# Kernel optimization log

Measured on AMD Instinct MI355X. Metric: run time of the kernel, lower is better.

## Reference

```python
import jax, jax.numpy as jnp
import numpy as np

B, T, IN, H = 64, 2048, 9, 128
FC1, OUT = 20, 1


def setup_inputs() -> dict:
    key = jax.random.key(0)
    ks = jax.random.split(key, 13)
    sh = 1.0 / np.sqrt(H)  # torch LSTM/Linear default init scale ~ U(-1/sqrt(H), 1/sqrt(H)); use gaussian of same magnitude
    s20 = 1.0 / np.sqrt(FC1)
    n = lambda k, shape, sc: (jax.random.normal(k, shape, jnp.float32) * sc)
    return {
        "x": jax.random.normal(ks[0], (B, T, IN), jnp.float32),
        # layer 0: W_ih [4H, IN], W_hh [4H, H]  (torch gate order: i, f, g, o)
        "W_ih0": n(ks[1], (4 * H, IN), sh),
        "W_hh0": n(ks[2], (4 * H, H), sh),
        "b_ih0": n(ks[3], (4 * H,), sh),
        "b_hh0": n(ks[4], (4 * H,), sh),
        # layer 1: input is h of layer 0 -> W_ih [4H, H]
        "W_ih1": n(ks[5], (4 * H, H), sh),
        "W_hh1": n(ks[6], (4 * H, H), sh),
        "b_ih1": n(ks[7], (4 * H,), sh),
        "b_hh1": n(ks[8], (4 * H,), sh),
        # head: fc1 (H->20), fc2 (20->1)
        "fc1_w": n(ks[9], (FC1, H), sh),
        "fc1_b": n(ks[10], (FC1,), sh),
        "fc2_w": n(ks[11], (OUT, FC1), s20),
        "fc2_b": n(ks[12], (OUT,), s20),
    }


def _lstm_layer(x, W_ih, W_hh, b_ih, b_hh):
    # x: [B, T, D_in] -> h_seq: [B, T, H]. Zero initial state (as in the module).
    b, t, _ = x.shape
    h_dim = W_hh.shape[1]
    # Precompute input-to-gate GEMM over all timesteps at once: [B, T, 4H]
    xg = jnp.einsum('btd,gd->btg', x, W_ih) + b_ih + b_hh

    def step(carry, g_t):  # g_t: [B, 4H]
        h, c = carry
        g = g_t + h @ W_hh.T
        i, f, gg, o = jnp.split(g, 4, axis=-1)
        i = jax.nn.sigmoid(i)
        f = jax.nn.sigmoid(f)
        gg = jnp.tanh(gg)
        o = jax.nn.sigmoid(o)
        c = f * c + i * gg
        h = o * jnp.tanh(c)
        return (h, c), h

    h0 = jnp.zeros((b, h_dim), x.dtype)
    c0 = jnp.zeros((b, h_dim), x.dtype)
    _, hs = jax.lax.scan(step, (h0, c0), jnp.swapaxes(xg, 0, 1))  # hs: [T, B, H]
    return jnp.swapaxes(hs, 0, 1)


def reference(x, W_ih0, W_hh0, b_ih0, b_hh0, W_ih1, W_hh1, b_ih1, b_hh1,
              fc1_w, fc1_b, fc2_w, fc2_b):
    out = _lstm_layer(x, W_ih0, W_hh0, b_ih0, b_hh0)
    out = _lstm_layer(out, W_ih1, W_hh1, b_ih1, b_hh1)
    # Per-timestep head fused into single batched GEMMs over all (B*T) rows.
    # Dropout(0.5) is identity in eval mode.
    h = jnp.tanh(out @ fc1_w.T + fc1_b)          # [B, T, 20]
    real_out = h @ fc2_w.T + fc2_b               # [B, T, 1]
    return real_out
```

## Files before the change

### kernel.cpp

```cpp
#include <hip/hip_runtime.h>
#include <hip/hip_bf16.h>

#define BATCH 64
#define TSEQ 2048
#define INF 9
#define H 128
#define G4 512
#define NFC 20
#define CH 64
#define NCH (TSEQ / CH)

__device__ __forceinline__ float sigf(float x) {
    return 1.0f / (1.0f + __expf(-x));
}
__device__ __forceinline__ float tanh_fast(float x) {
    return 1.0f - 2.0f / (__expf(2.0f * x) + 1.0f);
}

__device__ __forceinline__ void flag_release(int* f) {
    if (threadIdx.x == 0) {
        __threadfence();
        __hip_atomic_store(f, 1, __ATOMIC_RELEASE, __HIP_MEMORY_SCOPE_AGENT);
    }
}
__device__ __forceinline__ void flag_acquire(int* f) {
    if (threadIdx.x == 0) {
        while (__hip_atomic_load(f, __ATOMIC_ACQUIRE, __HIP_MEMORY_SCOPE_AGENT) == 0)
            __builtin_amdgcn_s_sleep(32);
        __threadfence();
    }
    __syncthreads();
}

__global__ __launch_bounds__(512) void zero_flags(int* flags, int n) {
    for (int i = threadIdx.x; i < n; i += 512) flags[i] = 0;
}

__global__ __launch_bounds__(512) void lstm_fused(
    const float* __restrict__ x,
    const float* __restrict__ Wih0, const float* __restrict__ Whh0,
    const float* __restrict__ bih0, const float* __restrict__ bhh0,
    const float* __restrict__ Wih1, const float* __restrict__ Whh1,
    const float* __restrict__ bih1, const float* __restrict__ bhh1,
    const float* __restrict__ fc1w, const float* __restrict__ fc1b,
    const float* __restrict__ fc2w, const float* __restrict__ fc2b,
    float* __restrict__ h0ring, float* __restrict__ xgring,
    int* __restrict__ fA, int* __restrict__ fAfree,
    int* __restrict__ fB, int* __restrict__ fBfree,
    int R, float* __restrict__ out)
{
    __shared__ float hs[H];
    __shared__ float gates[G4];
    __shared__ float hsB[2][H];
    __shared__ float hbuf[64][132];
    __shared__ float fc1w_s[NFC * 132];
    __shared__ float hfcb[64 * NFC];
    __shared__ float fc2w_s[NFC];
    __shared__ float fc1b_s[NFC];

    const int role = blockIdx.x >> 6;
    const int b    = blockIdx.x & 63;
    const int g    = threadIdx.x;

    if (role == 0) {
        float wih[INF], whh[H];
#pragma unroll
        for (int k = 0; k < INF; k++) wih[k] = Wih0[(size_t)g * INF + k];
        const float4* W4 = (const float4*)(Whh0 + (size_t)g * H);
#pragma unroll
        for (int k4 = 0; k4 < H / 4; k4++) {
            float4 wv = W4[k4];
            whh[4 * k4 + 0] = wv.x; whh[4 * k4 + 1] = wv.y;
            whh[4 * k4 + 2] = wv.z; whh[4 * k4 + 3] = wv.w;
        }
        const float bias = bih0[g] + bhh0[g];

        float c = 0.f;
        if (g < H) hs[g] = 0.f;

        const float* xb = x + (size_t)b * TSEQ * INF;
        float xr[INF];
#pragma unroll
        for (int k = 0; k < INF; k++) xr[k] = xb[k];
        __syncthreads();

        for (int ci = 0; ci < NCH; ci++) {
            if (ci >= R) flag_acquire(&fAfree[b * NCH + ci - R]);
            const int slot = ci % R;
            float* h0s = h0ring + ((size_t)slot * BATCH + b) * CH * H;

            for (int tt = 0; tt < CH; tt++) {
                const int t = ci * CH + tt;
                float a0 = bias, a1 = 0.f, a2 = 0.f, a3 = 0.f;
#pragma unroll
                for (int k = 0; k < INF; k++) a0 += wih[k] * xr[k];
                if (t + 1 < TSEQ) {
                    const float* xn = xb + (size_t)(t + 1) * INF;
#pragma unroll
                    for (int k = 0; k < INF; k++) xr[k] = xn[k];
                }
                const float4* h4 = (const float4*)hs;
#pragma unroll
                for (int k4 = 0; k4 < H / 4; k4++) {
                    float4 hv = h4[k4];
                    a0 += whh[4 * k4 + 0] * hv.x;
                    a1 += whh[4 * k4 + 1] * hv.y;
                    a2 += whh[4 * k4 + 2] * hv.z;
                    a3 += whh[4 * k4 + 3] * hv.w;
                }
                gates[g] = (a0 + a1) + (a2 + a3);
                __syncthreads();
                if (g < H) {
                    float ig = sigf(gates[g]);
                    float fg = sigf(gates[H + g]);
                    float gg = tanh_fast(gates[2 * H + g]);
                    float og = sigf(gates[3 * H + g]);
                    c = fg * c + ig * gg;
                    float h = og * tanh_fast(c);
                    hs[g] = h;
                    h0s[(size_t)tt * H + g] = h;
                }
                __syncthreads();
            }
            flag_release(&fA[b * NCH + ci]);
        }
    } else if (role == 1) {
        const float bias = bih1[g] + bhh1[g];
        const float4* W4 = (const float4*)(Wih1 + (size_t)g * H);

        for (int ci = 0; ci < NCH; ci++) {
            flag_acquire(&fA[b * NCH + ci]);
            if (ci >= R) flag_acquire(&fBfree[b * NCH + ci - R]);
            const int slot = ci % R;
            const float* h0s = h0ring + ((size_t)slot * BATCH + b) * CH * H;
            float* xgs = xgring + ((size_t)slot * BATCH + b) * CH * G4;

            for (int r2 = 0; r2 < CH / 2; r2++) {
                const int tt = 2 * r2;
                if (g < H)
                    hsB[0][g] = h0s[(size_t)tt * H + g];
                else if (g < 2 * H)
                    hsB[1][g - H] = h0s[(size_t)(tt + 1) * H + (g - H)];
                __syncthreads();
                float a0 = bias, a1 = 0.f, a2 = 0.f, a3 = 0.f;
                float c0 = bias, c1 = 0.f, c2 = 0.f, c3 = 0.f;
                const float4* h40 = (const float4*)hsB[0];
                const float4* h41 = (const float4*)hsB[1];
#pragma unroll
                for (int k4 = 0; k4 < H / 4; k4++) {
                    float4 wv = W4[k4];
                    float4 hv0 = h40[k4];
                    float4 hv1 = h41[k4];
                    a0 += wv.x * hv0.x; a1 += wv.y * hv0.y;
                    a2 += wv.z * hv0.z; a3 += wv.w * hv0.w;
                    c0 += wv.x * hv1.x; c1 += wv.y * hv1.y;
                    c2 += wv.z * hv1.z; c3 += wv.w * hv1.w;
                }
                xgs[(size_t)tt * G4 + g]       = (a0 + a1) + (a2 + a3);
                xgs[(size_t)(tt + 1) * G4 + g] = (c0 + c1) + (c2 + c3);
                __syncthreads();
            }
            flag_release(&fAfree[b * NCH + ci]);
            flag_release(&fB[b * NCH + ci]);
        }
    } else {
        float whh[H];
        const float4* W4 = (const float4*)(Whh1 + (size_t)g * H);
#pragma unroll
        for (int k4 = 0; k4 < H / 4; k4++) {
            float4 wv = W4[k4];
            whh[4 * k4 + 0] = wv.x; whh[4 * k4 + 1] = wv.y;
            whh[4 * k4 + 2] = wv.z; whh[4 * k4 + 3] = wv.w;
        }
        for (int i = g; i < NFC * H; i += 512) {
            int r = i >> 7, cidx = i & 127;
            fc1w_s[r * 132 + cidx] = fc1w[i];
        }
        if (g < NFC) { fc2w_s[g] = fc2w[g]; fc1b_s[g] = fc1b[g]; }

        float c = 0.f, h = 0.f;
        if (g < H) hs[g] = 0.f;
        const float fc2bias = fc2b[0];
        __syncthreads();

        for (int ci = 0; ci < NCH; ci++) {
            flag_acquire(&fB[b * NCH + ci]);
            const int slot = ci % R;
            const float* xgs = xgring + ((size_t)slot * BATCH + b) * CH * G4;
            float xgr = xgs[g];

            for (int tt = 0; tt < CH; tt++) {
                float a0 = xgr, a1 = 0.f, a2 = 0.f, a3 = 0.f;
                if (tt + 1 < CH) xgr = xgs[(size_t)(tt + 1) * G4 + g];
                const float4* h4 = (const float4*)hs;
#pragma unroll
                for (int k4 = 0; k4 < H / 4; k4++) {
                    float4 hv = h4[k4];
                    a0 += whh[4 * k4 + 0] * hv.x;
                    a1 += whh[4 * k4 + 1] * hv.y;
                    a2 += whh[4 * k4 + 2] * hv.z;
                    a3 += whh[4 * k4 + 3] * hv.w;
                }
                gates[g] = (a0 + a1) + (a2 + a3);
                __syncthreads();
                if (g < H) {
                    float ig = sigf(gates[g]);
                    float fg = sigf(gates[H + g]);
                    float gg = tanh_fast(gates[2 * H + g]);
                    float og = sigf(gates[3 * H + g]);
                    c = fg * c + ig * gg;
                    h = og * tanh_fast(c);
                    hs[g] = h;
                    hbuf[tt][g] = h;
                }
                __syncthreads();

                if (tt == CH - 1) {
#pragma unroll
                    for (int p = 0; p < 3; p++) {
                        int task = p * 512 + g;
                        if (task < 64 * NFC) {
                            int sidx = task / NFC;
                            int k = task - sidx * NFC;
                            float b0 = fc1b_s[k], b1 = 0.f, b2 = 0.f, b3 = 0.f;
                            const float4* hr = (const float4*)(&hbuf[sidx][0]);
                            const float4* wr = (const float4*)(&fc1w_s[k * 132]);
#pragma unroll
                            for (int k4 = 0; k4 < H / 4; k4++) {
                                float4 hv = hr[k4];
                                float4 wv = wr[k4];
                                b0 += wv.x * hv.x; b1 += wv.y * hv.y;
                                b2 += wv.z * hv.z; b3 += wv.w * hv.w;
                            }
                            hfcb[task] = tanh_fast((b0 + b1) + (b2 + b3));
                        }
                    }
                    __syncthreads();
                    if (g < 64) {
                        float o = fc2bias;
#pragma unroll
                        for (int k = 0; k < NFC; k++) o += fc2w_s[k] * hfcb[g * NFC + k];
                        out[(size_t)b * TSEQ + ci * CH + g] = o;
                    }
                    __syncthreads();
                }
            }
            flag_release(&fBfree[b * NCH + ci]);
        }
    }
}

__global__ __launch_bounds__(512, 2) void lstm0_scan(
    const float* __restrict__ x, const float* __restrict__ Wih,
    const float* __restrict__ Whh, const float* __restrict__ bih,
    const float* __restrict__ bhh, float* __restrict__ h0out)
{
    const int b = blockIdx.x;
    const int g = threadIdx.x;
    __shared__ float hs[H];
    __shared__ float gates[G4];
    float wih[INF], whh[H];
#pragma unroll
    for (int k = 0; k < INF; k++) wih[k] = Wih[(size_t)g * INF + k];
    const float4* W4 = (const float4*)(Whh + (size_t)g * H);
#pragma unroll
    for (int k4 = 0; k4 < H / 4; k4++) {
        float4 wv = W4[k4];
        whh[4 * k4 + 0] = wv.x; whh[4 * k4 + 1] = wv.y;
        whh[4 * k4 + 2] = wv.z; whh[4 * k4 + 3] = wv.w;
    }
    const float bias = bih[g] + bhh[g];
    float c = 0.f;
    if (g < H) hs[g] = 0.f;
    const float* xb = x + (size_t)b * TSEQ * INF;
    float xr[INF];
#pragma unroll
    for (int k = 0; k < INF; k++) xr[k] = xb[k];
    __syncthreads();
    for (int t = 0; t < TSEQ; t++) {
        float a0 = bias, a1 = 0.f, a2 = 0.f, a3 = 0.f;
#pragma unroll
        for (int k = 0; k < INF; k++) a0 += wih[k] * xr[k];
        if (t + 1 < TSEQ) {
            const float* xn = xb + (size_t)(t + 1) * INF;
#pragma unroll
            for (int k = 0; k < INF; k++) xr[k] = xn[k];
        }
        const float4* h4 = (const float4*)hs;
#pragma unroll
        for (int k4 = 0; k4 < H / 4; k4++) {
            float4 hv = h4[k4];
            a0 += whh[4 * k4 + 0] * hv.x;
            a1 += whh[4 * k4 + 1] * hv.y;
            a2 += whh[4 * k4 + 2] * hv.z;
            a3 += whh[4 * k4 + 3] * hv.w;
        }
        gates[g] = (a0 + a1) + (a2 + a3);
        __syncthreads();
        if (g < H) {
            float ig = sigf(gates[g]);
            float fg = sigf(gates[H + g]);
            float gg = tanh_fast(gates[2 * H + g]);
            float og = sigf(gates[3 * H + g]);
            c = fg * c + ig * gg;
            float h = og * tanh_fast(c);
            hs[g] = h;
            h0out[((size_t)b * TSEQ + t) * H + g] = h;
        }
        __syncthreads();
    }
}

__global__ __launch_bounds__(512, 2) void xg1_gemm(
    const float* __restrict__ h0, const float* __restrict__ Wih1,
    const float* __restrict__ bih, const float* __restrict__ bhh,
    float* __restrict__ xg1, int t0, int tlen)
{
    const int b = blockIdx.x >> 2;
    const int s = blockIdx.x & 3;
    const int g = threadIdx.x;
    const int rows = tlen >> 2;
    const int tstart = t0 + s * rows;
    float w[H];
    const float4* W4 = (const float4*)(Wih1 + (size_t)g * H);
#pragma unroll
    for (int k4 = 0; k4 < H / 4; k4++) {
        float4 wv = W4[k4];
        w[4 * k4 + 0] = wv.x; w[4 * k4 + 1] = wv.y;
        w[4 * k4 + 2] = wv.z; w[4 * k4 + 3] = wv.w;
    }
    const float bias = bih[g] + bhh[g];
    __shared__ float hs[2][H];
    if (g < H) hs[0][g] = h0[((size_t)b * TSEQ + tstart) * H + g];
    __syncthreads();
    for (int r = 0; r < rows; r++) {
        int buf = r & 1;
        if (g < H && (r + 1) < rows)
            hs[buf ^ 1][g] = h0[((size_t)b * TSEQ + tstart + r + 1) * H + g];
        float a0 = bias, a1 = 0.f, a2 = 0.f, a3 = 0.f;
        const float4* h4 = (const float4*)hs[buf];
#pragma unroll
        for (int k4 = 0; k4 < H / 4; k4++) {
            float4 hv = h4[k4];
            a0 += w[4 * k4 + 0] * hv.x;
            a1 += w[4 * k4 + 1] * hv.y;
            a2 += w[4 * k4 + 2] * hv.z;
            a3 += w[4 * k4 + 3] * hv.w;
        }
        xg1[((size_t)b * tlen + (size_t)(s * rows + r)) * G4 + g] = (a0 + a1) + (a2 + a3);
        __syncthreads();
    }
}

__global__ __launch_bounds__(512, 2) void lstm1_scan(
    const float* __restrict__ Whh1, const float* __restrict__ xg1,
    const float* __restrict__ fc1w, const float* __restrict__ fc1b,
    const float* __restrict__ fc2w, const float* __restrict__ fc2b,
    float* __restrict__ out, float* __restrict__ state, int t0, int tlen)
{
    const int b = blockIdx.x;
    const int g = threadIdx.x;
    __shared__ float hs[H];
    __shared__ float gates[G4];
    __shared__ float hbuf[64][132];
    __shared__ float fc1w_s[NFC * 132];
    __shared__ float hfcb[64 * NFC];
    __shared__ float fc2w_s[NFC];
    __shared__ float fc1b_s[NFC];
    float whh[H];
    const float4* W4 = (const float4*)(Whh1 + (size_t)g * H);
#pragma unroll
    for (int k4 = 0; k4 < H / 4; k4++) {
        float4 wv = W4[k4];
        whh[4 * k4 + 0] = wv.x; whh[4 * k4 + 1] = wv.y;
        whh[4 * k4 + 2] = wv.z; whh[4 * k4 + 3] = wv.w;
    }
    for (int i = g; i < NFC * H; i += 512) {
        int r = i >> 7, cidx = i & 127;
        fc1w_s[r * 132 + cidx] = fc1w[i];
    }
    if (g < NFC) { fc2w_s[g] = fc2w[g]; fc1b_s[g] = fc1b[g]; }
    float c = 0.f, h = 0.f;
    if (t0 > 0 && g < H) {
        c = state[b * H + g];
        h = state[BATCH * H + b * H + g];
    }
    if (g < H) hs[g] = h;
    float xgr = xg1[((size_t)b * tlen) * G4 + g];
    const float fc2bias = fc2b[0];
    __syncthreads();
    for (int tt = 0; tt < tlen; tt++) {
        float a0 = xgr, a1 = 0.f, a2 = 0.f, a3 = 0.f;
        if (tt + 1 < tlen) xgr = xg1[((size_t)b * tlen + tt + 1) * G4 + g];
        const float4* h4 = (const float4*)hs;
#pragma unroll
        for (int k4 = 0; k4 < H / 4; k4++) {
            float4 hv = h4[k4];
            a0 += whh[4 * k4 + 0] * hv.x;
            a1 += whh[4 * k4 + 1] * hv.y;
            a2 += whh[4 * k4 + 2] * hv.z;
            a3 += whh[4 * k4 + 3] * hv.w;
        }
        gates[g] = (a0 + a1) + (a2 + a3);
        __syncthreads();
        if (g < H) {
            float ig = sigf(gates[g]);
            float fg = sigf(gates[H + g]);
            float gg = tanh_fast(gates[2 * H + g]);
            float og = sigf(gates[3 * H + g]);
            c = fg * c + ig * gg;
            h = og * tanh_fast(c);
            hs[g] = h;
            hbuf[tt & 63][g] = h;
        }
        __syncthreads();
        if ((tt & 63) == 63) {
#pragma unroll
            for (int p = 0; p < 3; p++) {
                int task = p * 512 + g;
                if (task < 64 * NFC) {
                    int sidx = task / NFC;
                    int k = task - sidx * NFC;
                    float b0 = fc1b_s[k], b1 = 0.f, b2 = 0.f, b3 = 0.f;
                    const float4* hr = (const float4*)(&hbuf[sidx][0]);
                    const float4* wr = (const float4*)(&fc1w_s[k * 132]);
#pragma unroll
                    for (int k4 = 0; k4 < H / 4; k4++) {
                        float4 hv = hr[k4];
                        float4 wv = wr[k4];
                        b0 += wv.x * hv.x; b1 += wv.y * hv.y;
                        b2 += wv.z * hv.z; b3 += wv.w * hv.w;
                    }
                    hfcb[task] = tanh_fast((b0 + b1) + (b2 + b3));
                }
            }
            __syncthreads();
            if (g < 64) {
                float o = fc2bias;
#pragma unroll
                for (int k = 0; k < NFC; k++) o += fc2w_s[k] * hfcb[g * NFC + k];
                int tglob = t0 + tt - 63 + g;
                out[(size_t)b * TSEQ + tglob] = o;
            }
            __syncthreads();
        }
    }
    if (g < H) {
        state[b * H + g] = c;
        state[BATCH * H + b * H + g] = h;
    }
}

extern "C" void kernel_launch(void* const* d_in, const int* in_sizes, int n_in,
                              void* d_out, int out_size, void* d_ws, size_t ws_size,
                              hipStream_t stream) {
    const float* x    = (const float*)d_in[0];
    const float* Wih0 = (const float*)d_in[1];
    const float* Whh0 = (const float*)d_in[2];
    const float* bih0 = (const float*)d_in[3];
    const float* bhh0 = (const float*)d_in[4];
    const float* Wih1 = (const float*)d_in[5];
    const float* Whh1 = (const float*)d_in[6];
    const float* bih1 = (const float*)d_in[7];
    const float* bhh1 = (const float*)d_in[8];
    const float* fc1w = (const float*)d_in[9];
    const float* fc1b = (const float*)d_in[10];
    const float* fc2w = (const float*)d_in[11];
    const float* fc2b = (const float*)d_in[12];
    float* out = (float*)d_out;

    char* ws = (char*)d_ws;
    const size_t flag_region = 64 * 1024;
    const size_t h0slot = (size_t)BATCH * CH * H * 4;
    const size_t xgslot = (size_t)BATCH * CH * G4 * 4;

    int R = 0;
    if (ws_size > flag_region)
        R = (int)((ws_size - flag_region) / (h0slot + xgslot));
    if (R > NCH) R = NCH;

    if (R >= 2) {
        int* flags  = (int*)ws;
        int* fAp    = flags;
        int* fAfree = flags + BATCH * NCH;
        int* fBp    = flags + 2 * BATCH * NCH;
        int* fBfree = flags + 3 * BATCH * NCH;
        float* h0ring = (float*)(ws + flag_region);
        float* xgring = (float*)(ws + flag_region + h0slot * (size_t)R);

        zero_flags<<<1, 512, 0, stream>>>(flags, 4 * BATCH * NCH);
        lstm_fused<<<192, 512, 0, stream>>>(x, Wih0, Whh0, bih0, bhh0,
                                            Wih1, Whh1, bih1, bhh1,
                                            fc1w, fc1b, fc2w, fc2b,
                                            h0ring, xgring,
                                            fAp, fAfree, fBp, fBfree,
                                            R, out);
    } else {
        const size_t h0_bytes  = (size_t)BATCH * TSEQ * H * 4;
        const size_t mid_bytes = (size_t)2 * BATCH * H * 4;
        float* h0    = (float*)ws;
        float* state = (float*)(ws + h0_bytes);
        float* xg1   = (float*)(ws + h0_bytes + mid_bytes);
        int tlen = 64;
        const int cands[4] = {2048, 512, 128, 64};
        for (int i = 0; i < 4; i++) {
            size_t need = h0_bytes + mid_bytes + (size_t)BATCH * cands[i] * G4 * 4;
            if (ws_size >= need) { tlen = cands[i]; break; }
        }
        lstm0_scan<<<BATCH, 512, 0, stream>>>(x, Wih0, Whh0, bih0, bhh0, h0);
        const int nch = TSEQ / tlen;
        for (int ci = 0; ci < nch; ci++) {
            xg1_gemm<<<256, 512, 0, stream>>>(h0, Wih1, bih1, bhh1, xg1, ci * tlen, tlen);
            lstm1_scan<<<BATCH, 512, 0, stream>>>(Whh1, xg1, fc1w, fc1b, fc2w, fc2b,
                                                  out, state, ci * tlen, tlen);
        }
    }
}
```

Measured before the change: 3.417 ms.

## Halve pipeline chunk size, batch four timesteps in layer-1 input GEMM

Shrinks the chunk handed between the three pipelined roles from 64 to 32 timesteps, which shortens pipeline fill and drain latency at the cost of twice as many flag handshakes. The layer-1 input projection now processes four timesteps per weight load instead of two, improving weight reuse. Polling sleep is shortened, and the ready flag is released before the free flag so the consumer starts sooner. The head computation still runs every 64 timesteps, tracked by a global step counter, and the flag region and zeroing grid are enlarged to fit the doubled flag count.

```diff
diff --git a/kernel.cpp b/kernel.cpp
--- a/kernel.cpp
+++ b/kernel.cpp
@@ -7,7 +7,7 @@
 #define H 128
 #define G4 512
 #define NFC 20
-#define CH 64
+#define CH 32
 #define NCH (TSEQ / CH)
 
 __device__ __forceinline__ float sigf(float x) {
@@ -26,14 +26,15 @@
 __device__ __forceinline__ void flag_acquire(int* f) {
     if (threadIdx.x == 0) {
         while (__hip_atomic_load(f, __ATOMIC_ACQUIRE, __HIP_MEMORY_SCOPE_AGENT) == 0)
-            __builtin_amdgcn_s_sleep(32);
+            __builtin_amdgcn_s_sleep(2);
         __threadfence();
     }
     __syncthreads();
 }
 
 __global__ __launch_bounds__(512) void zero_flags(int* flags, int n) {
-    for (int i = threadIdx.x; i < n; i += 512) flags[i] = 0;
+    int i = blockIdx.x * 512 + threadIdx.x;
+    for (; i < n; i += gridDim.x * 512) flags[i] = 0;
 }
 
 __global__ __launch_bounds__(512) void lstm_fused(
@@ -51,7 +52,7 @@
 {
     __shared__ float hs[H];
     __shared__ float gates[G4];
-    __shared__ float hsB[2][H];
+    __shared__ float hsB4[4][H];
     __shared__ float hbuf[64][132];
     __shared__ float fc1w_s[NFC * 132];
     __shared__ float hfcb[64 * NFC];
@@ -135,33 +136,34 @@
             const float* h0s = h0ring + ((size_t)slot * BATCH + b) * CH * H;
             float* xgs = xgring + ((size_t)slot * BATCH + b) * CH * G4;
 
-            for (int r2 = 0; r2 < CH / 2; r2++) {
-                const int tt = 2 * r2;
-                if (g < H)
-                    hsB[0][g] = h0s[(size_t)tt * H + g];
-                else if (g < 2 * H)
-                    hsB[1][g - H] = h0s[(size_t)(tt + 1) * H + (g - H)];
+            for (int q = 0; q < CH / 4; q++) {
+                const int tt = 4 * q;
+                {
+                    int r = g >> 7;
+                    int k = g & 127;
+                    hsB4[r][k] = h0s[(size_t)(tt + r) * H + k];
+                }
                 __syncthreads();
-                float a0 = bias, a1 = 0.f, a2 = 0.f, a3 = 0.f;
-                float c0 = bias, c1 = 0.f, c2 = 0.f, c3 = 0.f;
-                const float4* h40 = (const float4*)hsB[0];
-                const float4* h41 = (const float4*)hsB[1];
+                float a0[4], a1[4], a2[4], a3[4];
+#pragma unroll
+                for (int r = 0; r < 4; r++) { a0[r] = bias; a1[r] = 0.f; a2[r] = 0.f; a3[r] = 0.f; }
 #pragma unroll
                 for (int k4 = 0; k4 < H / 4; k4++) {
                     float4 wv = W4[k4];
-                    float4 hv0 = h40[k4];
-                    float4 hv1 = h41[k4];
-                    a0 += wv.x * hv0.x; a1 += wv.y * hv0.y;
-                    a2 += wv.z * hv0.z; a3 += wv.w * hv0.w;
-                    c0 += wv.x * hv1.x; c1 += wv.y * hv1.y;
-                    c2 += wv.z * hv1.z; c3 += wv.w * hv1.w;
-                }
-                xgs[(size_t)tt * G4 + g]       = (a0 + a1) + (a2 + a3);
-                xgs[(size_t)(tt + 1) * G4 + g] = (c0 + c1) + (c2 + c3);
+#pragma unroll
+                    for (int r = 0; r < 4; r++) {
+                        float4 hv = ((const float4*)hsB4[r])[k4];
+                        a0[r] += wv.x * hv.x; a1[r] += wv.y * hv.y;
+                        a2[r] += wv.z * hv.z; a3[r] += wv.w * hv.w;
+                    }
+                }
+#pragma unroll
+                for (int r = 0; r < 4; r++)
+                    xgs[(size_t)(tt + r) * G4 + g] = (a0[r] + a1[r]) + (a2[r] + a3[r]);
                 __syncthreads();
             }
+            flag_release(&fB[b * NCH + ci]);
             flag_release(&fAfree[b * NCH + ci]);
-            flag_release(&fB[b * NCH + ci]);
         }
     } else {
         float whh[H];
@@ -190,6 +192,7 @@
             float xgr = xgs[g];
 
             for (int tt = 0; tt < CH; tt++) {
+                const int gt = ci * CH + tt;
                 float a0 = xgr, a1 = 0.f, a2 = 0.f, a3 = 0.f;
                 if (tt + 1 < CH) xgr = xgs[(size_t)(tt + 1) * G4 + g];
                 const float4* h4 = (const float4*)hs;
@@ -211,11 +214,11 @@
                     c = fg * c + ig * gg;
                     h = og * tanh_fast(c);
                     hs[g] = h;
-                    hbuf[tt][g] = h;
+                    hbuf[gt & 63][g] = h;
                 }
                 __syncthreads();
 
-                if (tt == CH - 1) {
+                if ((gt & 63) == 63) {
 #pragma unroll
                     for (int p = 0; p < 3; p++) {
                         int task = p * 512 + g;
@@ -240,7 +243,7 @@
                         float o = fc2bias;
 #pragma unroll
                         for (int k = 0; k < NFC; k++) o += fc2w_s[k] * hfcb[g * NFC + k];
-                        out[(size_t)b * TSEQ + ci * CH + g] = o;
+                        out[(size_t)b * TSEQ + gt - 63 + g] = o;
                     }
                     __syncthreads();
                 }
@@ -470,7 +473,7 @@
     float* out = (float*)d_out;
 
     char* ws = (char*)d_ws;
-    const size_t flag_region = 64 * 1024;
+    const size_t flag_region = 128 * 1024;
     const size_t h0slot = (size_t)BATCH * CH * H * 4;
     const size_t xgslot = (size_t)BATCH * CH * G4 * 4;
 
@@ -488,7 +491,7 @@
         float* h0ring = (float*)(ws + flag_region);
         float* xgring = (float*)(ws + flag_region + h0slot * (size_t)R);
 
-        zero_flags<<<1, 512, 0, stream>>>(flags, 4 * BATCH * NCH);
+        zero_flags<<<4, 512, 0, stream>>>(flags, 4 * BATCH * NCH);
         lstm_fused<<<192, 512, 0, stream>>>(x, Wih0, Whh0, bih0, bhh0,
                                             Wih1, Whh1, bih1, bhh1,
                                             fc1w, fc1b, fc2w, fc2b,
```

New measurement: 3.509 ms. +2.7%, slower.
